# Kernel optimization log

Hardware: AMD Instinct MI355X
Metric: run time of the kernel (lower is better)

## Reference

```python
import jax, jax.numpy as jnp
import numpy as np

B, M, N = 32, 1024, 1024

def setup_inputs() -> dict:
    key = jax.random.key(0)
    ks = jax.random.split(key, 7)
    return {
        "pred_r": jax.random.normal(ks[0], (B, M, 4), jnp.float32),
        "pred_t": jax.random.normal(ks[1], (B, M, 3), jnp.float32),
        "pred_c": jax.random.uniform(ks[2], (B, M), jnp.float32),
        "target": jax.random.normal(ks[3], (B, N, 3), jnp.float32),
        "model_points": jax.random.normal(ks[4], (B, N, 3), jnp.float32),
        "idx": jax.random.randint(ks[5], (B,), 0, 21),
        "points": jax.random.normal(ks[6], (B, M, 3), jnp.float32),
        "w": jnp.float32(0.015),
        "refine": 1,
    }

def quat_to_rotmat(q):
    # q: (B, M, 4) in xyzw order -> R: (B, M, 3, 3)
    q = q / (jnp.linalg.norm(q, axis=2, keepdims=True) + 1e-8)
    qx, qy, qz, qw = q[..., 0], q[..., 1], q[..., 2], q[..., 3]
    r1 = jnp.stack([1 - 2 * (qy * qy + qz * qz), 2 * (qx * qy - qz * qw), 2 * (qx * qz + qy * qw)], axis=-1)
    r2 = jnp.stack([2 * (qx * qy + qz * qw), 1 - 2 * (qx * qx + qz * qz), 2 * (qy * qz - qx * qw)], axis=-1)
    r3 = jnp.stack([2 * (qx * qz - qy * qw), 2 * (qy * qz + qx * qw), 1 - 2 * (qx * qx + qy * qy)], axis=-1)
    return jnp.stack([r1, r2, r3], axis=-2)

def reference(pred_r, pred_t, pred_c, target, model_points, idx, points, w, refine):
    # refine=True path (no symmetric-object KNN correspondence); idx/sym_list unused.
    pred_c = jnp.maximum(pred_c, 1e-6)                          # (B, M)
    R = quat_to_rotmat(pred_r)                                  # (B, M, 3, 3)
    # row-vector transform: mpR[b,m,n,j] = sum_i model_points[b,n,i] * R[b,m,i,j]
    mpR = jnp.einsum('bni,bmij->bmnj', model_points, R)         # (B, M, N, 3)
    pred_xyz = mpR + (points + pred_t)[:, :, None, :]           # (B, M, N, 3)
    diff = pred_xyz - target[:, None, :, :]
    dis_h = jnp.sqrt(jnp.sum(diff * diff, axis=-1)).mean(axis=2)  # (B, M)
    loss = jnp.mean(dis_h * pred_c - w * jnp.log(pred_c))
    which_max = jnp.argmax(pred_c, axis=1)                      # (B,)
    bidx = jnp.arange(B)
    R_best = R[bidx, which_max]                                 # (B, 3, 3)
    t_best = (points + pred_t)[bidx, which_max][:, None, :]     # (B, 1, 3)
    new_points = jnp.einsum('bmi,bij->bmj', points - t_best, R_best)
    new_target = jnp.einsum('bni,bij->bnj', target - t_best, R_best)
    dis_best = dis_h[bidx, which_max].mean()
    return (loss, dis_best,
            jax.lax.stop_gradient(new_points),
            jax.lax.stop_gradient(new_target))
```

## Files before the change

### kernel.cpp

```cpp
#include <hip/hip_runtime.h>

#define Bn 32
#define Mn 1024
#define Nn 1024

__device__ __forceinline__ float fsqrt(float x) { return __builtin_amdgcn_sqrtf(x); }

__device__ __forceinline__ void quat_to_R(float qx, float qy, float qz, float qw,
                                          float R[9]) {
    float norm = fsqrt(qx*qx + qy*qy + qz*qz + qw*qw) + 1e-8f;
    float inv = 1.0f / norm;
    float x = qx*inv, y = qy*inv, z = qz*inv, w = qw*inv;
    R[0] = 1.0f - 2.0f*(y*y + z*z);
    R[1] = 2.0f*(x*y - z*w);
    R[2] = 2.0f*(x*z + y*w);
    R[3] = 2.0f*(x*y + z*w);
    R[4] = 1.0f - 2.0f*(x*x + z*z);
    R[5] = 2.0f*(y*z - x*w);
    R[6] = 2.0f*(x*z - y*w);
    R[7] = 2.0f*(y*z + x*w);
    R[8] = 1.0f - 2.0f*(x*x + y*y);
}

__global__ __launch_bounds__(256) void k1_dis_loss(
    const float* __restrict__ pred_r, const float* __restrict__ pred_t,
    const float* __restrict__ pred_c, const float* __restrict__ target,
    const float* __restrict__ model_points, const float* __restrict__ points,
    const float* __restrict__ wptr,
    float* __restrict__ ws_loss,
    float* __restrict__ ws_amax,
    int*   __restrict__ ws_aidx,
    float* __restrict__ out)
{
    __shared__ __align__(16) float s[Nn * 8];
    __shared__ float red[256];

    const int b    = blockIdx.x >> 4;
    const int mc   = blockIdx.x & 15;
    const int tid  = threadIdx.x;
    const int lane = tid & 63;
    const int ng   = tid >> 6;

    if (blockIdx.x == 0 && tid == 0) out[1] = 0.0f;

    const float* mp_flat = model_points + b * Nn * 3;
    const float* tg_flat = target      + b * Nn * 3;
    for (int i = tid; i < Nn * 3; i += 256) {
        int n = i / 3;
        int r = i - n * 3;
        s[n * 8 + r]     = mp_flat[i];
        s[n * 8 + 3 + r] = tg_flat[i];
    }

    const int gm = b * Mn + mc * 64 + lane;
    float4 q = *(const float4*)(pred_r + gm * 4);
    float R[9];
    quat_to_R(q.x, q.y, q.z, q.w, R);
    const float tx = points[gm*3+0] + pred_t[gm*3+0];
    const float ty = points[gm*3+1] + pred_t[gm*3+1];
    const float tz = points[gm*3+2] + pred_t[gm*3+2];

    __syncthreads();

    float ssum = 0.0f;
    const int n0 = ng * 256;
    #pragma unroll 4
    for (int n = n0; n < n0 + 256; ++n) {
        const float* row = s + n * 8;
        float4 a  = *(const float4*)(row);
        float2 c2 = *(const float2*)(row + 4);
        float px = fmaf(a.x, R[0], fmaf(a.y, R[3], fmaf(a.z, R[6], tx)));
        float py = fmaf(a.x, R[1], fmaf(a.y, R[4], fmaf(a.z, R[7], ty)));
        float pz = fmaf(a.x, R[2], fmaf(a.y, R[5], fmaf(a.z, R[8], tz)));
        float dx = px - a.w;
        float dy = py - c2.x;
        float dz = pz - c2.y;
        ssum += fsqrt(fmaf(dx, dx, fmaf(dy, dy, dz * dz)));
    }

    red[tid] = ssum;
    __syncthreads();

    if (ng == 0) {
        float tot = red[lane] + red[lane + 64] + red[lane + 128] + red[lane + 192];
        float dis = tot * (1.0f / (float)Nn);
        float c = fmaxf(pred_c[gm], 1e-6f);
        float w = *wptr;
        float contrib = fmaf(dis, c, -w * logf(c));

        float av = c;
        int   ai = mc * 64 + lane;
        #pragma unroll
        for (int off = 32; off > 0; off >>= 1) {
            float ov = __shfl_xor(av, off);
            int   oi = __shfl_xor(ai, off);
            if (ov > av || (ov == av && oi < ai)) { av = ov; ai = oi; }
        }
        #pragma unroll
        for (int off = 32; off > 0; off >>= 1)
            contrib += __shfl_down(contrib, off);

        if (lane == 0) {
            ws_loss[blockIdx.x] = contrib;
            ws_amax[blockIdx.x] = av;
            ws_aidx[blockIdx.x] = ai;
        }
    }
}

__global__ __launch_bounds__(256) void k2_finalize(
    const float* __restrict__ pred_r, const float* __restrict__ pred_t,
    const float* __restrict__ target, const float* __restrict__ model_points,
    const float* __restrict__ points,
    const float* __restrict__ ws_loss, const float* __restrict__ ws_amax,
    const int* __restrict__ ws_aidx,
    float* __restrict__ out)
{
    const int b   = blockIdx.x >> 3;
    const int sl  = blockIdx.x & 7;
    const int tid = threadIdx.x;

    __shared__ float wredA[4];
    __shared__ float wredB[4];

    float bv = -1.0f; int bi = Mn;
    #pragma unroll
    for (int k = 0; k < 16; ++k) {
        float v = ws_amax[b * 16 + k];
        int   i = ws_aidx[b * 16 + k];
        if (v > bv || (v == bv && i < bi)) { bv = v; bi = i; }
    }
    const int gm = b * Mn + bi;
    float4 q = *(const float4*)(pred_r + gm * 4);
    float R[9];
    quat_to_R(q.x, q.y, q.z, q.w, R);
    const float tx = points[gm*3+0] + pred_t[gm*3+0];
    const float ty = points[gm*3+1] + pred_t[gm*3+1];
    const float tz = points[gm*3+2] + pred_t[gm*3+2];

    {
        const int t   = tid & 127;
        const int idx = sl * 128 + t;
        const bool is_p = (tid < 128);
        const float* src = is_p ? (points + (b * Mn + idx) * 3)
                                : (target + (b * Nn + idx) * 3);
        float* dst = is_p ? (out + 2 + (b * Mn + idx) * 3)
                          : (out + 2 + Bn * Mn * 3 + (b * Nn + idx) * 3);
        float x = src[0] - tx, y = src[1] - ty, z = src[2] - tz;
        dst[0] = fmaf(x, R[0], fmaf(y, R[3], z * R[6]));
        dst[1] = fmaf(x, R[1], fmaf(y, R[4], z * R[7]));
        dst[2] = fmaf(x, R[2], fmaf(y, R[5], z * R[8]));
    }

    float ssum = 0.0f;
    if (tid < 128) {
        const int n = sl * 128 + tid;
        const float* mp = model_points + (b * Nn + n) * 3;
        const float* tg = target      + (b * Nn + n) * 3;
        float px = fmaf(mp[0], R[0], fmaf(mp[1], R[3], fmaf(mp[2], R[6], tx)));
        float py = fmaf(mp[0], R[1], fmaf(mp[1], R[4], fmaf(mp[2], R[7], ty)));
        float pz = fmaf(mp[0], R[2], fmaf(mp[1], R[5], fmaf(mp[2], R[8], tz)));
        float dx = px - tg[0], dy = py - tg[1], dz = pz - tg[2];
        ssum = fsqrt(fmaf(dx, dx, fmaf(dy, dy, dz * dz)));
    }
    #pragma unroll
    for (int off = 32; off > 0; off >>= 1)
        ssum += __shfl_down(ssum, off);
    if ((tid & 63) == 0) wredA[tid >> 6] = ssum;
    __syncthreads();
    if (tid == 0) {
        float tot = wredA[0] + wredA[1] + wredA[2] + wredA[3];
        atomicAdd(out + 1, tot * (1.0f / ((float)Nn * (float)Bn)));
    }

    if (blockIdx.x == 0) {
        float ls = ws_loss[tid] + ws_loss[tid + 256];
        #pragma unroll
        for (int off = 32; off > 0; off >>= 1)
            ls += __shfl_down(ls, off);
        if ((tid & 63) == 0) wredB[tid >> 6] = ls;
        __syncthreads();
        if (tid == 0)
            out[0] = (wredB[0] + wredB[1] + wredB[2] + wredB[3])
                     * (1.0f / ((float)Bn * (float)Mn));
    }
}

extern "C" void kernel_launch(void* const* d_in, const int* in_sizes, int n_in,
                              void* d_out, int out_size, void* d_ws, size_t ws_size,
                              hipStream_t stream) {
    const float* pred_r       = (const float*)d_in[0];
    const float* pred_t       = (const float*)d_in[1];
    const float* pred_c       = (const float*)d_in[2];
    const float* target       = (const float*)d_in[3];
    const float* model_points = (const float*)d_in[4];
    const float* points       = (const float*)d_in[6];
    const float* wptr         = (const float*)d_in[7];

    float* out     = (float*)d_out;
    float* ws_loss = (float*)d_ws;
    float* ws_amax = ws_loss + 512;
    int*   ws_aidx = (int*)(ws_loss + 1024);

    k1_dis_loss<<<Bn * (Mn / 64), 256, 0, stream>>>(
        pred_r, pred_t, pred_c, target, model_points, points, wptr,
        ws_loss, ws_amax, ws_aidx, out);
    k2_finalize<<<8 * Bn, 256, 0, stream>>>(
        pred_r, pred_t, target, model_points, points,
        ws_loss, ws_amax, ws_aidx, out);
}
```

Measured before the change: 98.98 us.

## Fuse argmax and output transforms into main kernel, pack pairs for dual-FMA

Each block in the main kernel now computes the per-batch argmax of pred_c itself and writes the transformed points and targets for its slice. The best-row distance is taken from the already computed dis_h instead of being recomputed, which leaves the second kernel as a tiny single-block reduction. Shared memory is re-laid out so pairs of model points are handled with 2-wide vector FMAs, aiming at packed FP32 math in the hot loop. The cost is that every block redundantly scans 1024 pred_c values with an extra shared-memory reduction and several barriers.

```diff
diff --git a/kernel.cpp b/kernel.cpp
--- a/kernel.cpp
+++ b/kernel.cpp
@@ -4,7 +4,13 @@
 #define Mn 1024
 #define Nn 1024
 
+typedef float v2f __attribute__((ext_vector_type(2)));
+
 __device__ __forceinline__ float fsqrt(float x) { return __builtin_amdgcn_sqrtf(x); }
+__device__ __forceinline__ v2f fma2(v2f a, v2f b, v2f c) {
+    return __builtin_elementwise_fma(a, b, c);
+}
+__device__ __forceinline__ v2f splat(float x) { v2f v; v.x = x; v.y = x; return v; }
 
 __device__ __forceinline__ void quat_to_R(float qx, float qy, float qz, float qw,
                                           float R[9]) {
@@ -22,18 +28,19 @@
     R[8] = 1.0f - 2.0f*(x*x + y*y);
 }
 
-__global__ __launch_bounds__(256) void k1_dis_loss(
+__global__ __launch_bounds__(256) void k1_fused(
     const float* __restrict__ pred_r, const float* __restrict__ pred_t,
     const float* __restrict__ pred_c, const float* __restrict__ target,
     const float* __restrict__ model_points, const float* __restrict__ points,
     const float* __restrict__ wptr,
     float* __restrict__ ws_loss,
-    float* __restrict__ ws_amax,
-    int*   __restrict__ ws_aidx,
+    float* __restrict__ ws_dis,
     float* __restrict__ out)
 {
-    __shared__ __align__(16) float s[Nn * 8];
+    __shared__ __align__(16) float s[(Nn/2) * 12];
     __shared__ float red[256];
+    __shared__ float sval[256];
+    __shared__ int   sidx[256];
 
     const int b    = blockIdx.x >> 4;
     const int mc   = blockIdx.x & 15;
@@ -41,148 +48,143 @@
     const int lane = tid & 63;
     const int ng   = tid >> 6;
 
-    if (blockIdx.x == 0 && tid == 0) out[1] = 0.0f;
-
     const float* mp_flat = model_points + b * Nn * 3;
     const float* tg_flat = target      + b * Nn * 3;
     for (int i = tid; i < Nn * 3; i += 256) {
         int n = i / 3;
         int r = i - n * 3;
-        s[n * 8 + r]     = mp_flat[i];
-        s[n * 8 + 3 + r] = tg_flat[i];
+        int p = n >> 1;
+        int e = n & 1;
+        s[p * 12 + r * 2 + e]     = mp_flat[i];
+        s[p * 12 + 6 + r * 2 + e] = tg_flat[i];
     }
 
     const int gm = b * Mn + mc * 64 + lane;
     float4 q = *(const float4*)(pred_r + gm * 4);
     float R[9];
     quat_to_R(q.x, q.y, q.z, q.w, R);
-    const float tx = points[gm*3+0] + pred_t[gm*3+0];
-    const float ty = points[gm*3+1] + pred_t[gm*3+1];
-    const float tz = points[gm*3+2] + pred_t[gm*3+2];
+    const v2f sR0 = splat(R[0]), sR1 = splat(R[1]), sR2 = splat(R[2]);
+    const v2f sR3 = splat(R[3]), sR4 = splat(R[4]), sR5 = splat(R[5]);
+    const v2f sR6 = splat(R[6]), sR7 = splat(R[7]), sR8 = splat(R[8]);
+    const v2f tpx = splat(points[gm*3+0] + pred_t[gm*3+0]);
+    const v2f tpy = splat(points[gm*3+1] + pred_t[gm*3+1]);
+    const v2f tpz = splat(points[gm*3+2] + pred_t[gm*3+2]);
 
     __syncthreads();
 
-    float ssum = 0.0f;
-    const int n0 = ng * 256;
+    v2f acc = splat(0.0f);
+    const int p0 = ng * 128;
     #pragma unroll 4
-    for (int n = n0; n < n0 + 256; ++n) {
-        const float* row = s + n * 8;
-        float4 a  = *(const float4*)(row);
-        float2 c2 = *(const float2*)(row + 4);
-        float px = fmaf(a.x, R[0], fmaf(a.y, R[3], fmaf(a.z, R[6], tx)));
-        float py = fmaf(a.x, R[1], fmaf(a.y, R[4], fmaf(a.z, R[7], ty)));
-        float pz = fmaf(a.x, R[2], fmaf(a.y, R[5], fmaf(a.z, R[8], tz)));
-        float dx = px - a.w;
-        float dy = py - c2.x;
-        float dz = pz - c2.y;
-        ssum += fsqrt(fmaf(dx, dx, fmaf(dy, dy, dz * dz)));
-    }
-
-    red[tid] = ssum;
+    for (int p = p0; p < p0 + 128; ++p) {
+        const float* row = s + p * 12;
+        float4 A  = *(const float4*)(row);
+        float4 Bq = *(const float4*)(row + 4);
+        float4 Cq = *(const float4*)(row + 8);
+        v2f mx; mx.x = A.x;  mx.y = A.y;
+        v2f my; my.x = A.z;  my.y = A.w;
+        v2f mz; mz.x = Bq.x; mz.y = Bq.y;
+        v2f Tx; Tx.x = Bq.z; Tx.y = Bq.w;
+        v2f Ty; Ty.x = Cq.x; Ty.y = Cq.y;
+        v2f Tz; Tz.x = Cq.z; Tz.y = Cq.w;
+        v2f px = fma2(mx, sR0, fma2(my, sR3, fma2(mz, sR6, tpx)));
+        v2f py = fma2(mx, sR1, fma2(my, sR4, fma2(mz, sR7, tpy)));
+        v2f pz = fma2(mx, sR2, fma2(my, sR5, fma2(mz, sR8, tpz)));
+        v2f dx = px - Tx;
+        v2f dy = py - Ty;
+        v2f dz = pz - Tz;
+        v2f d2 = fma2(dx, dx, fma2(dy, dy, dz * dz));
+        v2f sr; sr.x = fsqrt(d2.x); sr.y = fsqrt(d2.y);
+        acc += sr;
+    }
+
+    red[tid] = acc.x + acc.y;
     __syncthreads();
 
+    float dis = 0.0f;
     if (ng == 0) {
         float tot = red[lane] + red[lane + 64] + red[lane + 128] + red[lane + 192];
-        float dis = tot * (1.0f / (float)Nn);
+        dis = tot * (1.0f / (float)Nn);
         float c = fmaxf(pred_c[gm], 1e-6f);
         float w = *wptr;
         float contrib = fmaf(dis, c, -w * logf(c));
-
-        float av = c;
-        int   ai = mc * 64 + lane;
-        #pragma unroll
-        for (int off = 32; off > 0; off >>= 1) {
-            float ov = __shfl_xor(av, off);
-            int   oi = __shfl_xor(ai, off);
-            if (ov > av || (ov == av && oi < ai)) { av = ov; ai = oi; }
-        }
         #pragma unroll
         for (int off = 32; off > 0; off >>= 1)
             contrib += __shfl_down(contrib, off);
-
-        if (lane == 0) {
+        if (lane == 0)
             ws_loss[blockIdx.x] = contrib;
-            ws_amax[blockIdx.x] = av;
-            ws_aidx[blockIdx.x] = ai;
+    }
+
+    {
+        float bv = -1.0f; int bi = 0;
+        #pragma unroll
+        for (int k = 0; k < 4; ++k) {
+            int m = k * 256 + tid;
+            float v = fmaxf(pred_c[b * Mn + m], 1e-6f);
+            if (v > bv) { bv = v; bi = m; }
         }
-    }
-}
-
-__global__ __launch_bounds__(256) void k2_finalize(
-    const float* __restrict__ pred_r, const float* __restrict__ pred_t,
-    const float* __restrict__ target, const float* __restrict__ model_points,
-    const float* __restrict__ points,
-    const float* __restrict__ ws_loss, const float* __restrict__ ws_amax,
-    const int* __restrict__ ws_aidx,
+        sval[tid] = bv; sidx[tid] = bi;
+        __syncthreads();
+        for (int off = 128; off > 0; off >>= 1) {
+            if (tid < off) {
+                float v2 = sval[tid + off]; int i2 = sidx[tid + off];
+                if (v2 > sval[tid] || (v2 == sval[tid] && i2 < sidx[tid])) {
+                    sval[tid] = v2; sidx[tid] = i2;
+                }
+            }
+            __syncthreads();
+        }
+    }
+    const int best = sidx[0];
+
+    if (ng == 0 && (best >> 6) == mc && lane == (best & 63))
+        ws_dis[b] = dis;
+
+    if (tid < 128) {
+        const int t    = tid & 63;
+        const int idx  = mc * 64 + t;
+        const bool isp = (tid < 64);
+        const int gb = b * Mn + best;
+        float4 qb = *(const float4*)(pred_r + gb * 4);
+        float Rb[9];
+        quat_to_R(qb.x, qb.y, qb.z, qb.w, Rb);
+        const float btx = points[gb*3+0] + pred_t[gb*3+0];
+        const float bty = points[gb*3+1] + pred_t[gb*3+1];
+        const float btz = points[gb*3+2] + pred_t[gb*3+2];
+        const float* src = isp ? (points + (b * Mn + idx) * 3)
+                               : (target + (b * Nn + idx) * 3);
+        float* dst = isp ? (out + 2 + (b * Mn + idx) * 3)
+                         : (out + 2 + Bn * Mn * 3 + (b * Nn + idx) * 3);
+        float x = src[0] - btx, y = src[1] - bty, z = src[2] - btz;
+        dst[0] = fmaf(x, Rb[0], fmaf(y, Rb[3], z * Rb[6]));
+        dst[1] = fmaf(x, Rb[1], fmaf(y, Rb[4], z * Rb[7]));
+        dst[2] = fmaf(x, Rb[2], fmaf(y, Rb[5], z * Rb[8]));
+    }
+}
+
+__global__ __launch_bounds__(256) void k2_reduce(
+    const float* __restrict__ ws_loss, const float* __restrict__ ws_dis,
     float* __restrict__ out)
 {
-    const int b   = blockIdx.x >> 3;
-    const int sl  = blockIdx.x & 7;
     const int tid = threadIdx.x;
-
-    __shared__ float wredA[4];
-    __shared__ float wredB[4];
-
-    float bv = -1.0f; int bi = Mn;
-    #pragma unroll
-    for (int k = 0; k < 16; ++k) {
-        float v = ws_amax[b * 16 + k];
-        int   i = ws_aidx[b * 16 + k];
-        if (v > bv || (v == bv && i < bi)) { bv = v; bi = i; }
-    }
-    const int gm = b * Mn + bi;
-    float4 q = *(const float4*)(pred_r + gm * 4);
-    float R[9];
-    quat_to_R(q.x, q.y, q.z, q.w, R);
-    const float tx = points[gm*3+0] + pred_t[gm*3+0];
-    const float ty = points[gm*3+1] + pred_t[gm*3+1];
-    const float tz = points[gm*3+2] + pred_t[gm*3+2];
-
-    {
-        const int t   = tid & 127;
-        const int idx = sl * 128 + t;
-        const bool is_p = (tid < 128);
-        const float* src = is_p ? (points + (b * Mn + idx) * 3)
-                                : (target + (b * Nn + idx) * 3);
-        float* dst = is_p ? (out + 2 + (b * Mn + idx) * 3)
-                          : (out + 2 + Bn * Mn * 3 + (b * Nn + idx) * 3);
-        float x = src[0] - tx, y = src[1] - ty, z = src[2] - tz;
-        dst[0] = fmaf(x, R[0], fmaf(y, R[3], z * R[6]));
-        dst[1] = fmaf(x, R[1], fmaf(y, R[4], z * R[7]));
-        dst[2] = fmaf(x, R[2], fmaf(y, R[5], z * R[8]));
-    }
-
-    float ssum = 0.0f;
-    if (tid < 128) {
-        const int n = sl * 128 + tid;
-        const float* mp = model_points + (b * Nn + n) * 3;
-        const float* tg = target      + (b * Nn + n) * 3;
-        float px = fmaf(mp[0], R[0], fmaf(mp[1], R[3], fmaf(mp[2], R[6], tx)));
-        float py = fmaf(mp[0], R[1], fmaf(mp[1], R[4], fmaf(mp[2], R[7], ty)));
-        float pz = fmaf(mp[0], R[2], fmaf(mp[1], R[5], fmaf(mp[2], R[8], tz)));
-        float dx = px - tg[0], dy = py - tg[1], dz = pz - tg[2];
-        ssum = fsqrt(fmaf(dx, dx, fmaf(dy, dy, dz * dz)));
-    }
+    __shared__ float wred[4];
+
+    float ls = ws_loss[tid] + ws_loss[tid + 256];
     #pragma unroll
     for (int off = 32; off > 0; off >>= 1)
-        ssum += __shfl_down(ssum, off);
-    if ((tid & 63) == 0) wredA[tid >> 6] = ssum;
+        ls += __shfl_down(ls, off);
+    if ((tid & 63) == 0) wred[tid >> 6] = ls;
     __syncthreads();
-    if (tid == 0) {
-        float tot = wredA[0] + wredA[1] + wredA[2] + wredA[3];
-        atomicAdd(out + 1, tot * (1.0f / ((float)Nn * (float)Bn)));
-    }
-
-    if (blockIdx.x == 0) {
-        float ls = ws_loss[tid] + ws_loss[tid + 256];
+    if (tid == 0)
+        out[0] = (wred[0] + wred[1] + wred[2] + wred[3])
+                 * (1.0f / ((float)Bn * (float)Mn));
+
+    if (tid < 64) {
+        float dv = (tid < Bn) ? ws_dis[tid] : 0.0f;
         #pragma unroll
         for (int off = 32; off > 0; off >>= 1)
-            ls += __shfl_down(ls, off);
-        if ((tid & 63) == 0) wredB[tid >> 6] = ls;
-        __syncthreads();
+            dv += __shfl_down(dv, off);
         if (tid == 0)
-            out[0] = (wredB[0] + wredB[1] + wredB[2] + wredB[3])
-                     * (1.0f / ((float)Bn * (float)Mn));
+            out[1] = dv * (1.0f / (float)Bn);
     }
 }
 
@@ -199,13 +201,10 @@
 
     float* out     = (float*)d_out;
     float* ws_loss = (float*)d_ws;
-    float* ws_amax = ws_loss + 512;
-    int*   ws_aidx = (int*)(ws_loss + 1024);
-
-    k1_dis_loss<<<Bn * (Mn / 64), 256, 0, stream>>>(
+    float* ws_dis  = ws_loss + 512;
+
+    k1_fused<<<Bn * (Mn / 64), 256, 0, stream>>>(
         pred_r, pred_t, pred_c, target, model_points, points, wptr,
-        ws_loss, ws_amax, ws_aidx, out);
-    k2_finalize<<<8 * Bn, 256, 0, stream>>>(
-        pred_r, pred_t, target, model_points, points,
-        ws_loss, ws_amax, ws_aidx, out);
-}
+        ws_loss, ws_dis, out);
+    k2_reduce<<<1, 256, 0, stream>>>(ws_loss, ws_dis, out);
+}
```

Result: faster. 92.39 us (-6.7%).
